# Kernel optimization log

Measured on AMD Instinct MI355X. Metric: run time of the kernel, lower is better.

## Reference

```python
import jax, jax.numpy as jnp
import numpy as np

N, IN, SEG, OUT = 2048, 32, 16, 64


def setup_inputs() -> dict:
    key = jax.random.key(0)
    k1, k2 = jax.random.split(key)
    x_in = jax.random.normal(k1, (N, IN), dtype=jnp.float32)
    # x param: sorted breakpoints per (in, out) pair, as in custom_init(linspace)
    x_param = jnp.broadcast_to(
        jnp.linspace(-3.0, 3.0, SEG + 1, dtype=jnp.float32)[None, :, None],
        (IN, SEG + 1, OUT),
    ).copy()
    y_param = jax.random.normal(k2, (IN, SEG + 1, OUT), dtype=jnp.float32)
    return {"x_in": x_in, "x_param": x_param, "y_param": y_param}


def reference(x_in, x_param, y_param):
    # x_in: [N, IN]; x_param/y_param: [IN, SEG+1, OUT]
    xe = x_in[:, :, None, None]                 # [N, IN, 1, 1]
    x_lo = x_param[:, :-1, :]                   # [IN, SEG, OUT]
    x_hi = x_param[:, 1:, :]
    # dense segment-membership mask, [N, IN, SEG, OUT]
    mask = (xe < x_hi) & (xe >= x_lo)
    # below-range -> first segment; above-range -> last segment
    mask = mask.at[:, :, 0:1, :].set(mask[:, :, 0:1, :] | (xe < x_param[:, 0:1, :]))
    mask = mask.at[:, :, -1:, :].set(mask[:, :, -1:, :] | (xe >= x_param[:, -1:, :]))
    divider = x_hi - x_lo
    divider = jnp.where(divider == 0.0, jnp.float32(1e-4), divider)
    ratio = (y_param[:, 1:, :] - y_param[:, :-1, :]) / divider  # slope per segment
    m = mask.astype(x_in.dtype)
    # two-point formula, masked to the active segment
    ypred = m * (ratio * (xe - x_lo) + y_param[:, :-1, :])      # [N, IN, SEG, OUT]
    return jnp.sum(ypred, axis=(1, 2))                          # [N, OUT]
```

## Files before the change

### kernel.cpp

```cpp
#include <hip/hip_runtime.h>

#define PN   2048
#define PIN  32
#define PSEG 16
#define POUT 64

#define NT   4

__global__ __launch_bounds__(64) void prep_kernel(
    const float* __restrict__ xp, const float* __restrict__ yp,
    float2* __restrict__ table, float* __restrict__ bp)
{
    const int i = blockIdx.x;
    const int s = blockIdx.y;
    const int o = threadIdx.x;
    const size_t base = ((size_t)i * (PSEG + 1) + s) * POUT + o;
    const float lo  = xp[base];
    const float hi  = xp[base + POUT];
    const float ylo = yp[base];
    const float yhi = yp[base + POUT];
    float d = hi - lo;
    d = (d == 0.0f) ? 1e-4f : d;
    const float slope = (yhi - ylo) / d;
    const float c     = fmaf(-slope, lo, ylo);
    table[((size_t)i * PSEG + s) * POUT + o] = make_float2(slope, c);
    if (o == 0) {
        bp[i * (PSEG + 1) + s] = lo;
        if (s == PSEG - 1) bp[i * (PSEG + 1) + PSEG] = hi;
    }
}

__global__ __launch_bounds__(256) void seg_main(
    const float* __restrict__ x_in,
    const float2* __restrict__ table,
    const float* __restrict__ bp,
    float* __restrict__ out)
{
    const int o     = threadIdx.x & 63;
    const int w     = threadIdx.x >> 6;
    const int nbase = (int)blockIdx.x * NT;

    __shared__ float xs[NT * PIN];
    __shared__ float bps[PIN * (PSEG + 1)];
    __shared__ int   segs[NT * PIN];

    if (threadIdx.x < NT * PIN) {
        const int n_l = threadIdx.x >> 5;
        const int i_l = threadIdx.x & 31;
        xs[threadIdx.x] = x_in[(nbase + n_l) * PIN + i_l];
    }
    for (int t = threadIdx.x; t < PIN * (PSEG + 1); t += 256) bps[t] = bp[t];
    __syncthreads();

    if (threadIdx.x < NT * PIN) {
        const int n_l = threadIdx.x >> 5;
        const int i_l = threadIdx.x & 31;
        const float x = xs[threadIdx.x];
        const float* b = &bps[i_l * (PSEG + 1)];
        int seg = 0;
#pragma unroll
        for (int s = 1; s <= PSEG; ++s) seg += (x >= b[s]) ? 1 : 0;
        seg = min(seg, PSEG - 1);
        segs[threadIdx.x] = seg;
    }
    __syncthreads();

    float accA = 0.0f, accB = 0.0f;
    float accC = 0.0f, accD = 0.0f;
#pragma unroll
    for (int i = 0; i < PIN; i += 2) {
        const int   s0 = segs[w * PIN + i];
        const float x0 = xs[w * PIN + i];
        const int   s1 = segs[w * PIN + i + 1];
        const float x1 = xs[w * PIN + i + 1];
        const float2 sc0 = table[((size_t)(i    ) * PSEG + s0) * POUT + o];
        const float2 sc1 = table[((size_t)(i + 1) * PSEG + s1) * POUT + o];
        accA = fmaf(sc0.x, x0, accA);
        accB += sc0.y;
        accC = fmaf(sc1.x, x1, accC);
        accD += sc1.y;
    }
    out[(size_t)(nbase + w) * POUT + o] = (accA + accB) + (accC + accD);
}

extern "C" void kernel_launch(void* const* d_in, const int* in_sizes, int n_in,
                              void* d_out, int out_size, void* d_ws, size_t ws_size,
                              hipStream_t stream)
{
    const float* x_in = (const float*)d_in[0];
    const float* xp   = (const float*)d_in[1];
    const float* yp   = (const float*)d_in[2];
    float* out        = (float*)d_out;

    float2* table = (float2*)d_ws;
    float*  bp    = (float*)((char*)d_ws + (size_t)PIN * PSEG * POUT * sizeof(float2));

    prep_kernel<<<dim3(PIN, PSEG), dim3(64), 0, stream>>>(xp, yp, table, bp);
    seg_main<<<dim3(PN / NT), dim3(256), 0, stream>>>(x_in, table, bp, out);
}
```

Before: 64.29 us.

## Move segment search into prep kernel and split each row's reduction across waves

The prep kernel now also computes per-(row,input) table offsets in extra blocks, reading breakpoints directly from xp, so the segment search leaves the main kernel. The main kernel gives each row its own block, has the four waves each handle eight inputs, and combines their partial sums through shared memory. This raises parallelism from 512 to 2048 blocks and shortens each thread's dependent gather chain. In exchange it adds a global offset buffer round trip, an extra barrier, and more block launches.

```diff
diff --git a/kernel.cpp b/kernel.cpp
--- a/kernel.cpp
+++ b/kernel.cpp
@@ -5,82 +5,81 @@
 #define PSEG 16
 #define POUT 64
 
-#define NT   4
+#define TABLE_ELEMS (PIN * PSEG * POUT)
 
-__global__ __launch_bounds__(64) void prep_kernel(
+__global__ __launch_bounds__(256) void prep_kernel(
+    const float* __restrict__ x_in,
     const float* __restrict__ xp, const float* __restrict__ yp,
-    float2* __restrict__ table, float* __restrict__ bp)
+    float2* __restrict__ table, int* __restrict__ off)
 {
-    const int i = blockIdx.x;
-    const int s = blockIdx.y;
-    const int o = threadIdx.x;
-    const size_t base = ((size_t)i * (PSEG + 1) + s) * POUT + o;
-    const float lo  = xp[base];
-    const float hi  = xp[base + POUT];
-    const float ylo = yp[base];
-    const float yhi = yp[base + POUT];
-    float d = hi - lo;
-    d = (d == 0.0f) ? 1e-4f : d;
-    const float slope = (yhi - ylo) / d;
-    const float c     = fmaf(-slope, lo, ylo);
-    table[((size_t)i * PSEG + s) * POUT + o] = make_float2(slope, c);
-    if (o == 0) {
-        bp[i * (PSEG + 1) + s] = lo;
-        if (s == PSEG - 1) bp[i * (PSEG + 1) + PSEG] = hi;
+    if (blockIdx.x < 128) {
+        const int g = blockIdx.x * 256 + threadIdx.x;
+        const int o = g & 63;
+        const int s = (g >> 6) & 15;
+        const int i = g >> 10;
+        const size_t base = ((size_t)i * (PSEG + 1) + s) * POUT + o;
+        const float lo  = xp[base];
+        const float hi  = xp[base + POUT];
+        const float ylo = yp[base];
+        const float yhi = yp[base + POUT];
+        float d = hi - lo;
+        d = (d == 0.0f) ? 1e-4f : d;
+        const float slope = (yhi - ylo) / d;
+        table[g] = make_float2(slope, fmaf(-slope, lo, ylo));
+    } else {
+        const int b = blockIdx.x - 128;
+        __shared__ float bps[PIN * (PSEG + 1)];
+        for (int t = threadIdx.x; t < PIN * (PSEG + 1); t += 256)
+            bps[t] = xp[(size_t)t * POUT];
+        __syncthreads();
+        const int i = threadIdx.x & 31;
+        const int n = b * 8 + (threadIdx.x >> 5);
+        const float x = x_in[n * PIN + i];
+        const float* bpr = &bps[i * (PSEG + 1)];
+        int seg = 0;
+#pragma unroll
+        for (int s = 1; s <= PSEG; ++s) seg += (x >= bpr[s]) ? 1 : 0;
+        seg = min(seg, PSEG - 1);
+        off[n * PIN + i] = (i * PSEG + seg) * POUT;
     }
 }
 
 __global__ __launch_bounds__(256) void seg_main(
     const float* __restrict__ x_in,
     const float2* __restrict__ table,
-    const float* __restrict__ bp,
+    const int* __restrict__ off,
     float* __restrict__ out)
 {
-    const int o     = threadIdx.x & 63;
-    const int w     = threadIdx.x >> 6;
-    const int nbase = (int)blockIdx.x * NT;
+    const int n = blockIdx.x;
+    const int o = threadIdx.x & 63;
+    const int w = threadIdx.x >> 6;
 
-    __shared__ float xs[NT * PIN];
-    __shared__ float bps[PIN * (PSEG + 1)];
-    __shared__ int   segs[NT * PIN];
+    __shared__ float xs[PIN];
+    __shared__ int   offs[PIN];
+    __shared__ float red[4 * 64];
 
-    if (threadIdx.x < NT * PIN) {
-        const int n_l = threadIdx.x >> 5;
-        const int i_l = threadIdx.x & 31;
-        xs[threadIdx.x] = x_in[(nbase + n_l) * PIN + i_l];
-    }
-    for (int t = threadIdx.x; t < PIN * (PSEG + 1); t += 256) bps[t] = bp[t];
+    if (threadIdx.x < PIN)
+        xs[threadIdx.x] = x_in[n * PIN + threadIdx.x];
+    else if (threadIdx.x < 2 * PIN)
+        offs[threadIdx.x - PIN] = off[n * PIN + (threadIdx.x - PIN)];
     __syncthreads();
 
-    if (threadIdx.x < NT * PIN) {
-        const int n_l = threadIdx.x >> 5;
-        const int i_l = threadIdx.x & 31;
-        const float x = xs[threadIdx.x];
-        const float* b = &bps[i_l * (PSEG + 1)];
-        int seg = 0;
+    float a0 = 0.0f, a1 = 0.0f, a2 = 0.0f, a3 = 0.0f;
 #pragma unroll
-        for (int s = 1; s <= PSEG; ++s) seg += (x >= b[s]) ? 1 : 0;
-        seg = min(seg, PSEG - 1);
-        segs[threadIdx.x] = seg;
+    for (int k = 0; k < 8; k += 2) {
+        const int i0 = w * 8 + k, i1 = i0 + 1;
+        const float2 sc0 = table[offs[i0] + o];
+        const float2 sc1 = table[offs[i1] + o];
+        a0 = fmaf(sc0.x, xs[i0], a0);
+        a1 += sc0.y;
+        a2 = fmaf(sc1.x, xs[i1], a2);
+        a3 += sc1.y;
     }
+    red[w * 64 + o] = (a0 + a1) + (a2 + a3);
     __syncthreads();
 
-    float accA = 0.0f, accB = 0.0f;
-    float accC = 0.0f, accD = 0.0f;
-#pragma unroll
-    for (int i = 0; i < PIN; i += 2) {
-        const int   s0 = segs[w * PIN + i];
-        const float x0 = xs[w * PIN + i];
-        const int   s1 = segs[w * PIN + i + 1];
-        const float x1 = xs[w * PIN + i + 1];
-        const float2 sc0 = table[((size_t)(i    ) * PSEG + s0) * POUT + o];
-        const float2 sc1 = table[((size_t)(i + 1) * PSEG + s1) * POUT + o];
-        accA = fmaf(sc0.x, x0, accA);
-        accB += sc0.y;
-        accC = fmaf(sc1.x, x1, accC);
-        accD += sc1.y;
-    }
-    out[(size_t)(nbase + w) * POUT + o] = (accA + accB) + (accC + accD);
+    if (threadIdx.x < 64)
+        out[(size_t)n * POUT + o] = (red[o] + red[64 + o]) + (red[128 + o] + red[192 + o]);
 }
 
 extern "C" void kernel_launch(void* const* d_in, const int* in_sizes, int n_in,
@@ -93,8 +92,8 @@
     float* out        = (float*)d_out;
 
     float2* table = (float2*)d_ws;
-    float*  bp    = (float*)((char*)d_ws + (size_t)PIN * PSEG * POUT * sizeof(float2));
+    int*    off   = (int*)((char*)d_ws + (size_t)TABLE_ELEMS * sizeof(float2));
 
-    prep_kernel<<<dim3(PIN, PSEG), dim3(64), 0, stream>>>(xp, yp, table, bp);
-    seg_main<<<dim3(PN / NT), dim3(256), 0, stream>>>(x_in, table, bp, out);
+    prep_kernel<<<dim3(384), dim3(256), 0, stream>>>(x_in, xp, yp, table, off);
+    seg_main<<<dim3(PN), dim3(256), 0, stream>>>(x_in, table, off, out);
 }
```

Measured after the change: 61.79 us. -3.9%, faster.
